# Optimization experiments

Measured on AMD Instinct MI355X. Metric: run time of the kernel, lower is better.

## Reference

```python
import jax, jax.numpy as jnp
import numpy as np

T, HID, H, KV, D = 2048, 2048, 16, 8, 128
EPS = 1e-6
THETA = 10000.0


def setup_inputs() -> dict:
    key = jax.random.key(0)
    ks = jax.random.split(key, 6)
    positions = jnp.arange(T, dtype=jnp.int64 if jax.config.jax_enable_x64 else jnp.int32)
    hidden_states = jax.random.normal(ks[0], (T, HID), dtype=jnp.float32)
    scale = 0.02
    Wq = jax.random.normal(ks[1], (HID, H * 2 * D), dtype=jnp.float32) * scale
    Wk = jax.random.normal(ks[2], (HID, KV * D), dtype=jnp.float32) * scale
    Wv = jax.random.normal(ks[3], (HID, KV * D), dtype=jnp.float32) * scale
    Wo = jax.random.normal(ks[4], (H * D, HID), dtype=jnp.float32) * scale
    q_norm_w = jnp.zeros((D,), dtype=jnp.float32)  # torch init: zeros, applied as (1+w)
    k_norm_w = jnp.zeros((D,), dtype=jnp.float32)
    return {"positions": positions, "hidden_states": hidden_states, "Wq": Wq,
            "Wk": Wk, "Wv": Wv, "Wo": Wo, "q_norm_w": q_norm_w, "k_norm_w": k_norm_w}


def _rms_norm(x, w):
    # fp32 RMSNorm with (1 + weight) scaling, per last dim
    xf = x.astype(jnp.float32)
    inv = jax.lax.rsqrt(jnp.mean(xf * xf, axis=-1, keepdims=True) + EPS)
    return (xf * inv * (1.0 + w.astype(jnp.float32))).astype(x.dtype)


def _rope(x, positions):
    # neox-style rotary over full head_dim; x: (T, heads, D)
    half = D // 2
    inv_freq = 1.0 / (THETA ** (jnp.arange(0, half, dtype=jnp.float32) / half))
    freqs = positions.astype(jnp.float32)[:, None] * inv_freq  # (T, half)
    cos = jnp.cos(freqs)[:, None, :]  # (T,1,half)
    sin = jnp.sin(freqs)[:, None, :]
    x1, x2 = x[..., :half], x[..., half:]
    return jnp.concatenate([x1 * cos - x2 * sin, x2 * cos + x1 * sin], axis=-1)


def reference(positions, hidden_states, Wq, Wk, Wv, Wo, q_norm_w, k_norm_w):
    scaling = D ** -0.5
    qg = (hidden_states @ Wq).reshape(T, H, 2 * D)
    q, gate = qg[..., :D], qg[..., D:]              # (T,H,D) each
    k = (hidden_states @ Wk).reshape(T, KV, D)
    v = (hidden_states @ Wv).reshape(T, KV, D)
    q = _rms_norm(q, q_norm_w)
    k = _rms_norm(k, k_norm_w)
    q = _rope(q, positions)
    k = _rope(k, positions)
    # GQA: repeat kv heads
    rep = H // KV
    k = jnp.repeat(k, rep, axis=1)                   # (T,H,D)
    v = jnp.repeat(v, rep, axis=1)
    scores = jnp.einsum('thd,shd->hts', q, k) * scaling  # (H,T,T)
    causal = positions[:, None] >= positions[None, :]     # (T,T)
    scores = jnp.where(causal[None], scores, jnp.finfo(scores.dtype).min)
    probs = jax.nn.softmax(scores, axis=-1)
    o = jnp.einsum('hts,shd->thd', probs, v).reshape(T, H * D)
    o = o * jax.nn.sigmoid(gate.reshape(T, H * D))
    return o @ Wo
```

## Files before the change

kernel.cpp:

```cpp
#include <hip/hip_runtime.h>
#include <stdint.h>
#include <math.h>

#define T_SEQ 2048
#define HID   2048
#define NH    16
#define NKV   8
#define DH    128

typedef __bf16 bf16x8 __attribute__((ext_vector_type(8)));
typedef float  f32x4  __attribute__((ext_vector_type(4)));

__device__ __forceinline__ ushort f2bf(float f) {
  uint32_t u = __float_as_uint(f);
  u += 0x7FFF + ((u >> 16) & 1);
  return (ushort)(u >> 16);
}
__device__ __forceinline__ ushort f2bf_rz(float f) {
  return (ushort)(__float_as_uint(f) >> 16);
}
__device__ __forceinline__ float bf2f(ushort u) {
  return __uint_as_float(((uint32_t)u) << 16);
}
__device__ __forceinline__ void gld16(const void* g, void* l) {
  __builtin_amdgcn_global_load_lds(
      (const __attribute__((address_space(1))) uint32_t*)g,
      (__attribute__((address_space(3))) uint32_t*)l, 16, 0, 0);
}

__global__ __launch_bounds__(256) void prep_kernel(
    const float* __restrict__ hs, const float* __restrict__ Wq,
    const float* __restrict__ Wk, const float* __restrict__ Wv,
    const float* __restrict__ Wo, ushort* __restrict__ hs16,
    ushort* __restrict__ Wqt, ushort* __restrict__ Wkt,
    ushort* __restrict__ Wvt, ushort* __restrict__ Wot) {
  int bid = blockIdx.x;
  if (bid < 4096) {
    int i = (bid * 256 + threadIdx.x) * 4;
    float4 v = *(const float4*)(hs + i);
    ushort4 o = {f2bf(v.x), f2bf(v.y), f2bf(v.z), f2bf(v.w)};
    *(ushort4*)(hs16 + i) = o;
    return;
  }
  bid -= 4096;
  const float* src; ushort* dst; int N, bi, bj;
  if (bid < 2048)      { src = Wq; dst = Wqt; N = 4096; bj = bid & 63; bi = bid >> 6; }
  else if (bid < 2560) { bid -= 2048; src = Wk; dst = Wkt; N = 1024; bj = bid & 15; bi = bid >> 4; }
  else if (bid < 3072) { bid -= 2560; src = Wv; dst = Wvt; N = 1024; bj = bid & 15; bi = bid >> 4; }
  else                 { bid -= 3072; src = Wo; dst = Wot; N = 2048; bj = bid & 31; bi = bid >> 5; }
  __shared__ float tile[64][65];
  const int r = threadIdx.x >> 2, cg = (threadIdx.x & 3) * 16;
  const float* sp = src + (size_t)(bi * 64 + r) * N + bj * 64 + cg;
#pragma unroll
  for (int p = 0; p < 4; ++p) {
    float4 v = *(const float4*)(sp + p * 4);
    tile[r][cg + p * 4 + 0] = v.x; tile[r][cg + p * 4 + 1] = v.y;
    tile[r][cg + p * 4 + 2] = v.z; tile[r][cg + p * 4 + 3] = v.w;
  }
  __syncthreads();
  ushort* dp = dst + (size_t)(bj * 64 + r) * HID + bi * 64 + cg;
#pragma unroll
  for (int p = 0; p < 2; ++p) {
    union { uint4 v; ushort u[8]; } o;
#pragma unroll
    for (int j = 0; j < 8; ++j) o.u[j] = f2bf(tile[cg + p * 8 + j][r]);
    *(uint4*)(dp + p * 8) = o.v;
  }
}

template <int MI>
__device__ __forceinline__ void gemm_loop(
    const ushort* __restrict__ A, const ushort* __restrict__ Bt,
    int K, int m0, int n0, ushort* As, ushort* Bs, f32x4 (*acc)[4]) {
  const int tid = threadIdx.x, lane = tid & 63, w = tid >> 6;
  const int quad = lane >> 4, l15 = lane & 15;
  const int wm = (w >> 1) * (MI * 16), wn = (w & 1) * 64;
  const int srow = tid >> 2, sch = tid & 3;
  for (int k0 = 0; k0 < K; k0 += 32) {
    __syncthreads();
#pragma unroll
    for (int p = 0; p < MI / 2; ++p) {
      int row = p * 64 + srow;
      int gch = sch ^ ((row >> 1) & 3);
      gld16(A + (size_t)(m0 + row) * K + k0 + gch * 8,
            As + (p * 256 + w * 64) * 8);
    }
#pragma unroll
    for (int p = 0; p < 2; ++p) {
      int row = p * 64 + srow;
      int gch = sch ^ ((row >> 1) & 3);
      gld16(Bt + (size_t)(n0 + row) * K + k0 + gch * 8,
            Bs + (p * 256 + w * 64) * 8);
    }
    __syncthreads();
    bf16x8 af[MI], bfr[4];
#pragma unroll
    for (int mi = 0; mi < MI; ++mi) {
      int row = wm + mi * 16 + l15;
      int pch = quad ^ ((row >> 1) & 3);
      af[mi] = *(const bf16x8*)(As + row * 32 + pch * 8);
    }
#pragma unroll
    for (int ni = 0; ni < 4; ++ni) {
      int row = wn + ni * 16 + l15;
      int pch = quad ^ ((row >> 1) & 3);
      bfr[ni] = *(const bf16x8*)(Bs + row * 32 + pch * 8);
    }
#pragma unroll
    for (int mi = 0; mi < MI; ++mi)
#pragma unroll
      for (int ni = 0; ni < 4; ++ni)
        acc[mi][ni] = __builtin_amdgcn_mfma_f32_16x16x32_bf16(
            af[mi], bfr[ni], acc[mi][ni], 0, 0, 0);
  }
}

__device__ __forceinline__ void bf16_store(f32x4 (*acc)[4],
                                           ushort* __restrict__ Cb, int Ncols,
                                           int m0, int n0) {
  const int lane = threadIdx.x & 63, w = threadIdx.x >> 6;
  const int quad = lane >> 4, l15 = lane & 15;
  const int wm = (w >> 1) * 64, wn = (w & 1) * 64;
#pragma unroll
  for (int mi = 0; mi < 4; ++mi)
#pragma unroll
    for (int ni = 0; ni < 4; ++ni)
#pragma unroll
      for (int r = 0; r < 4; ++r) {
        int row = m0 + wm + mi * 16 + quad * 4 + r;
        int col = n0 + wn + ni * 16 + l15;
        Cb[(size_t)row * Ncols + col] = f2bf(acc[mi][ni][r]);
      }
}

struct SmemQKV {
  union {
    struct { ushort As[128 * 32]; ushort Bs[128 * 32]; } g;
    struct { ushort qn[128][132]; float rss[128][2]; } n;
  };
};

__device__ __forceinline__ void norm_rope_store(
    f32x4 (*acc)[4], ushort* __restrict__ dst, int nheads, int m0, int head,
    const int* __restrict__ positions, const float* __restrict__ wgt,
    SmemQKV* sm) {
  const int tid = threadIdx.x, lane = tid & 63, w = tid >> 6;
  const int quad = lane >> 4, l15 = lane & 15;
  const int wm = (w >> 1) * 64, wn = (w & 1) * 64;
  __syncthreads();
#pragma unroll
  for (int mi = 0; mi < 4; ++mi)
#pragma unroll
    for (int r = 0; r < 4; ++r) {
      const int row = wm + mi * 16 + quad * 4 + r;
      float ss = 0.f;
#pragma unroll
      for (int ni = 0; ni < 4; ++ni) {
        float v = acc[mi][ni][r];
        ss += v * v;
        sm->n.qn[row][wn + ni * 16 + l15] = f2bf(v);
      }
      ss += __shfl_xor(ss, 8, 64);
      ss += __shfl_xor(ss, 4, 64);
      ss += __shfl_xor(ss, 2, 64);
      ss += __shfl_xor(ss, 1, 64);
      if (l15 == 0) sm->n.rss[row][w & 1] = ss;
    }
  __syncthreads();
  const int row = tid >> 1, d0 = (tid & 1) * 32;
  const int t = m0 + row;
  const float rstd =
      rsqrtf((sm->n.rss[row][0] + sm->n.rss[row][1]) * (1.f / 128.f) + 1e-6f);
  const float pos = (float)positions[t];
  ushort o1[32], o2[32];
#pragma unroll
  for (int j = 0; j < 32; ++j) {
    const int d = d0 + j;
    float x1 = bf2f(sm->n.qn[row][d]) * rstd * (1.f + wgt[d]);
    float x2 = bf2f(sm->n.qn[row][d + 64]) * rstd * (1.f + wgt[d + 64]);
    float rev = pos * exp2f((float)d * -0.20762050593045233f) *
                0.15915494309189535f;
    float fr = rev - floorf(rev);
    float s = __builtin_amdgcn_sinf(fr);
    float c = __builtin_amdgcn_cosf(fr);
    o1[j] = f2bf(x1 * c - x2 * s);
    o2[j] = f2bf(x2 * c + x1 * s);
  }
  ushort* op = dst + ((size_t)t * nheads + head) * DH;
#pragma unroll
  for (int p = 0; p < 4; ++p)
    *(uint4*)(op + d0 + p * 8) = *(const uint4*)(o1 + p * 8);
#pragma unroll
  for (int p = 0; p < 4; ++p)
    *(uint4*)(op + 64 + d0 + p * 8) = *(const uint4*)(o2 + p * 8);
}

__global__ __launch_bounds__(256) void gemm_qkv(
    const ushort* __restrict__ hs16, const ushort* __restrict__ Wqt,
    const ushort* __restrict__ Wkt, const ushort* __restrict__ Wvt,
    const int* __restrict__ positions, const float* __restrict__ qnw,
    const float* __restrict__ knw, ushort* __restrict__ q16,
    ushort* __restrict__ gate16, ushort* __restrict__ k16,
    ushort* __restrict__ v16t) {
  __shared__ alignas(16) SmemQKV sm;
  f32x4 acc[4][4];
#pragma unroll
  for (int i = 0; i < 4; ++i)
#pragma unroll
    for (int j = 0; j < 4; ++j) acc[i][j] = (f32x4){0.f, 0.f, 0.f, 0.f};
  const int b = blockIdx.x;
  if (b < 512) {
    int mt = b >> 5, nt = b & 31, m0 = mt * 128;
    gemm_loop<4>(hs16, Wqt, HID, m0, nt * 128, sm.g.As, sm.g.Bs, acc);
    if ((nt & 1) == 0)
      norm_rope_store(acc, q16, NH, m0, nt >> 1, positions, qnw, &sm);
    else
      bf16_store(acc, gate16, NH * DH, m0, (nt >> 1) * 128);
  } else if (b < 640) {
    int f = b - 512, m0 = (f >> 3) * 128, n0 = (f & 7) * 128;
    gemm_loop<4>(hs16, Wkt, HID, m0, n0, sm.g.As, sm.g.Bs, acc);
    norm_rope_store(acc, k16, NKV, m0, n0 >> 7, positions, knw, &sm);
  } else {
    int f = b - 640, m0 = (f >> 4) * 128, n0 = (f & 15) * 128;
    gemm_loop<4>(Wvt, hs16, HID, m0, n0, sm.g.As, sm.g.Bs, acc);
    bf16_store(acc, v16t, T_SEQ, m0, n0);
  }
}

__global__ __launch_bounds__(256) void gemm_out(
    const ushort* __restrict__ ob16, const ushort* __restrict__ Wot,
    float* __restrict__ out) {
  __shared__ ushort As[64 * 32];
  __shared__ ushort Bs[128 * 32];
  f32x4 acc[2][4];
#pragma unroll
  for (int i = 0; i < 2; ++i)
#pragma unroll
    for (int j = 0; j < 4; ++j) acc[i][j] = (f32x4){0.f, 0.f, 0.f, 0.f};
  const int b = blockIdx.x;
  const int m0 = (b >> 4) * 64, n0 = (b & 15) * 128;
  gemm_loop<2>(ob16, Wot, HID, m0, n0, As, Bs, acc);
  const int lane = threadIdx.x & 63, w = threadIdx.x >> 6;
  const int quad = lane >> 4, l15 = lane & 15;
  const int wm = (w >> 1) * 32, wn = (w & 1) * 64;
#pragma unroll
  for (int mi = 0; mi < 2; ++mi)
#pragma unroll
    for (int ni = 0; ni < 4; ++ni)
#pragma unroll
      for (int r = 0; r < 4; ++r) {
        int row = m0 + wm + mi * 16 + quad * 4 + r;
        int col = n0 + wn + ni * 16 + l15;
        out[(size_t)row * HID + col] = acc[mi][ni][r];
      }
}

__global__ __launch_bounds__(256) void attn_mfma(
    const ushort* __restrict__ q16, const ushort* __restrict__ k16,
    const ushort* __restrict__ v16t, const float* __restrict__ qnw,
    const float* __restrict__ knw, ushort* __restrict__ Op0,
    ushort* __restrict__ Op1, ushort* __restrict__ Op2,
    float* __restrict__ lpart) {
  const int pb = blockIdx.x, h = blockIdx.y, s = blockIdx.z, kvh = h >> 1;
  const int tid = threadIdx.x, lane = tid & 63, w = tid >> 6;
  const int quad = lane >> 4, l15 = lane & 15;

  __shared__ ushort Ks[64 * 128];
  __shared__ ushort Vs[144 * 64];
  __shared__ ushort Ps[4][16][72];

  for (int i = tid; i < 16 * 64; i += 256) {
    int row = 128 + (i >> 6), col = i & 63;
    Vs[row * 64 + col] = (row == 128) ? (ushort)0x3F80 : (ushort)0;
  }

  __shared__ float s8[8];
  __shared__ float bshare;
  {
    float mq = 0.f, mk = 0.f;
    if (tid < 128) { mq = fabsf(1.f + qnw[tid]); mk = fabsf(1.f + knw[tid]); }
#pragma unroll
    for (int off = 32; off >= 1; off >>= 1) {
      mq = fmaxf(mq, __shfl_xor(mq, off, 64));
      mk = fmaxf(mk, __shfl_xor(mk, off, 64));
    }
    if (lane == 0) { s8[w * 2] = mq; s8[w * 2 + 1] = mk; }
    __syncthreads();
    if (tid == 0) {
      float MQ = fmaxf(s8[0], s8[2]), MK = fmaxf(s8[1], s8[3]);
      bshare = 16.3217f * MQ * MK * 1.02f + 0.1f;
    }
    __syncthreads();
  }
  const float B = bshare;
  const float CSC = 0.08838834764831845f * 1.44269504088896f;

#pragma unroll 1
  for (int sel = 0; sel < 2; ++sel) {
    const int qt = sel ? (31 - pb) : pb;
    const int q0 = qt * 64;
    const int ntl = (qt >= s) ? ((qt - s) / 3 + 1) : 0;

    bf16x8 qf[4];
    const ushort* qbase = q16 + ((size_t)(q0 + w * 16 + l15) * NH + h) * DH;
#pragma unroll
    for (int ks = 0; ks < 4; ++ks)
      qf[ks] = *(const bf16x8*)(qbase + ks * 32 + quad * 8);

    f32x4 oacc[9];
#pragma unroll
    for (int i = 0; i < 9; ++i) oacc[i] = (f32x4){0.f, 0.f, 0.f, 0.f};

#pragma unroll 1
    for (int it = 0; it < ntl; ++it) {
      const int kt = s + 3 * it;
      const int kt0 = kt * 64;
      __syncthreads();
#pragma unroll
      for (int p = 0; p < 4; ++p) {
        int row = p * 16 + (tid >> 4), ch = tid & 15;
        int gch = ch ^ (row & 15);
        gld16(k16 + ((size_t)(kt0 + row) * NKV + kvh) * DH + gch * 8,
              Ks + (p * 256 + w * 64) * 8);
      }
#pragma unroll
      for (int p = 0; p < 4; ++p) {
        int row = p * 32 + (tid >> 3), ch = tid & 7;
        int gch = ch ^ (row & 7);
        gld16(v16t + (size_t)(kvh * DH + row) * T_SEQ + kt0 + gch * 8,
              Vs + (p * 256 + w * 64) * 8);
      }
      __syncthreads();

      f32x4 sacc[4];
#pragma unroll
      for (int ni = 0; ni < 4; ++ni) sacc[ni] = (f32x4){0.f, 0.f, 0.f, 0.f};
#pragma unroll
      for (int ks = 0; ks < 4; ++ks)
#pragma unroll
        for (int ni = 0; ni < 4; ++ni) {
          int row = ni * 16 + l15;
          int pch = (ks * 4 + quad) ^ (row & 15);
          bf16x8 kf = *(const bf16x8*)(Ks + row * 128 + pch * 8);
          sacc[ni] = __builtin_amdgcn_mfma_f32_16x16x32_bf16(
              qf[ks], kf, sacc[ni], 0, 0, 0);
        }

      const bool diag = (kt == qt);
#pragma unroll
      for (int ni = 0; ni < 4; ++ni) {
        int key = kt0 + ni * 16 + l15;
#pragma unroll
        for (int r = 0; r < 4; ++r) {
          float arg = fmaf(sacc[ni][r], CSC, -B);
          float pv;
          if (diag) {
            int q = q0 + w * 16 + quad * 4 + r;
            pv = (key <= q) ? exp2f(arg) : 0.f;
          } else {
            pv = exp2f(arg);
          }
          Ps[w][quad * 4 + r][ni * 16 + l15] = f2bf_rz(pv);
        }
      }

#pragma unroll
      for (int ks2 = 0; ks2 < 2; ++ks2) {
        bf16x8 pf = *(const bf16x8*)(&Ps[w][l15][ks2 * 32 + quad * 8]);
#pragma unroll
        for (int ni = 0; ni < 9; ++ni) {
          int row = ni * 16 + l15;
          int pch = (ks2 * 4 + quad) ^ (row & 7);
          bf16x8 vf = *(const bf16x8*)(Vs + row * 64 + pch * 8);
          oacc[ni] = __builtin_amdgcn_mfma_f32_16x16x32_bf16(
              pf, vf, oacc[ni], 0, 0, 0);
        }
      }
    }

    ushort* Op = (s == 0) ? Op0 : (s == 1) ? Op1 : Op2;
#pragma unroll
    for (int ni = 0; ni < 8; ++ni) {
      int d = ni * 16 + l15;
#pragma unroll
      for (int r = 0; r < 4; ++r) {
        int q = q0 + w * 16 + quad * 4 + r;
        Op[((size_t)h * T_SEQ + q) * DH + d] = f2bf(oacc[ni][r]);
      }
    }
    if (l15 == 0) {
#pragma unroll
      for (int r = 0; r < 4; ++r) {
        int q = q0 + w * 16 + quad * 4 + r;
        lpart[(size_t)s * (NH * T_SEQ) + h * T_SEQ + q] = oacc[8][r];
      }
    }
  }
}

__global__ __launch_bounds__(256) void combine_kernel(
    const ushort* __restrict__ Op0, const ushort* __restrict__ Op1,
    const ushort* __restrict__ Op2, const float* __restrict__ lpart,
    const ushort* __restrict__ gate16, ushort* __restrict__ ob16) {
  const int t = blockIdx.x, tid = threadIdx.x;
  const int h = tid >> 4, d0 = (tid & 15) * 8;
  const int NT = NH * T_SEQ;
  const float l = lpart[h * T_SEQ + t] + lpart[NT + h * T_SEQ + t] +
                  lpart[2 * NT + h * T_SEQ + t];
  const float inv = 1.0f / l;
  const size_t po = ((size_t)h * T_SEQ + t) * DH + d0;
  ushort4 a0 = *(const ushort4*)(Op0 + po);
  ushort4 a1 = *(const ushort4*)(Op0 + po + 4);
  ushort4 b0 = *(const ushort4*)(Op1 + po);
  ushort4 b1 = *(const ushort4*)(Op1 + po + 4);
  ushort4 c0 = *(const ushort4*)(Op2 + po);
  ushort4 c1 = *(const ushort4*)(Op2 + po + 4);
  const ushort* gp = gate16 + (size_t)t * (NH * DH) + h * DH + d0;
  ushort4 g0 = *(const ushort4*)(gp);
  ushort4 g1 = *(const ushort4*)(gp + 4);
  float oa[8] = {bf2f(a0.x), bf2f(a0.y), bf2f(a0.z), bf2f(a0.w),
                 bf2f(a1.x), bf2f(a1.y), bf2f(a1.z), bf2f(a1.w)};
  float ob[8] = {bf2f(b0.x), bf2f(b0.y), bf2f(b0.z), bf2f(b0.w),
                 bf2f(b1.x), bf2f(b1.y), bf2f(b1.z), bf2f(b1.w)};
  float oc[8] = {bf2f(c0.x), bf2f(c0.y), bf2f(c0.z), bf2f(c0.w),
                 bf2f(c1.x), bf2f(c1.y), bf2f(c1.z), bf2f(c1.w)};
  float gg[8] = {bf2f(g0.x), bf2f(g0.y), bf2f(g0.z), bf2f(g0.w),
                 bf2f(g1.x), bf2f(g1.y), bf2f(g1.z), bf2f(g1.w)};
  ushort r[8];
#pragma unroll
  for (int i = 0; i < 8; ++i) {
    float o = (oa[i] + ob[i] + oc[i]) * inv;
    o = o / (1.0f + exp2f(-gg[i] * 1.44269504088896f));
    r[i] = f2bf(o);
  }
  ushort* op = ob16 + (size_t)t * (NH * DH) + h * DH + d0;
  *(ushort4*)(op)     = (ushort4){r[0], r[1], r[2], r[3]};
  *(ushort4*)(op + 4) = (ushort4){r[4], r[5], r[6], r[7]};
}

extern "C" void kernel_launch(void* const* d_in, const int* in_sizes, int n_in,
                              void* d_out, int out_size, void* d_ws, size_t ws_size,
                              hipStream_t stream) {
  const int*   positions = (const int*)d_in[0];
  const float* hs  = (const float*)d_in[1];
  const float* Wq  = (const float*)d_in[2];
  const float* Wk  = (const float*)d_in[3];
  const float* Wv  = (const float*)d_in[4];
  const float* Wo  = (const float*)d_in[5];
  const float* qnw = (const float*)d_in[6];
  const float* knw = (const float*)d_in[7];
  float* out = (float*)d_out;

  const size_t MB = 1 << 20;
  uint8_t* ws = (uint8_t*)d_ws;
  ushort* hs16  = (ushort*)(ws + 0);
  ushort* Op0   = (ushort*)(ws + 0);
  ushort* Wqt   = (ushort*)(ws + 8 * MB);
  ushort* Op1   = (ushort*)(ws + 8 * MB);
  ushort* Op2   = (ushort*)(ws + 16 * MB);
  ushort* Wkt   = (ushort*)(ws + 24 * MB);
  ushort* ob16  = (ushort*)(ws + 24 * MB);
  ushort* Wvt   = (ushort*)(ws + 28 * MB);
  ushort* v16t  = (ushort*)(ws + 32 * MB);
  ushort* k16   = (ushort*)(ws + 36 * MB);
  ushort* q16   = (ushort*)(ws + 40 * MB);
  ushort* gate16= (ushort*)(ws + 48 * MB);
  ushort* Wot   = (ushort*)(ws + 56 * MB);
  float*  lpart = (float*)d_out;

  prep_kernel<<<8192, 256, 0, stream>>>(hs, Wq, Wk, Wv, Wo,
                                        hs16, Wqt, Wkt, Wvt, Wot);
  gemm_qkv<<<768, 256, 0, stream>>>(hs16, Wqt, Wkt, Wvt, positions, qnw, knw,
                                    q16, gate16, k16, v16t);
  attn_mfma<<<dim3(16, NH, 3), 256, 0, stream>>>(q16, k16, v16t, qnw, knw,
                                                 Op0, Op1, Op2, lpart);
  combine_kernel<<<T_SEQ, 256, 0, stream>>>(Op0, Op1, Op2, lpart, gate16, ob16);
  gemm_out<<<512, 256, 0, stream>>>(ob16, Wot, out);
}
```

Measured before the change: 291.4 us.

## Fuse RMSNorm+RoPE in registers via 4x1 warp tiling; widen out-GEMM K tile

The Q/K projection GEMM now uses a 4x1 warp layout, so each wave holds whole 128-wide head rows. RMSNorm and RoPE can then run directly in registers with 16-lane shuffles, with no shared-memory staging and no extra block barriers. The output GEMM gets its own inline loop with a 64-wide K tile and XOR swizzle, halving the barrier count per K. Costs: each wave reloads the full B tile per k-step (less reuse), stores become scattered 2-byte writes instead of 16-byte vector writes, and shared memory for gemm_out grows.

```diff
diff --git a/kernel.cpp b/kernel.cpp
--- a/kernel.cpp
+++ b/kernel.cpp
@@ -133,66 +133,111 @@
       }
 }
 
-struct SmemQKV {
-  union {
-    struct { ushort As[128 * 32]; ushort Bs[128 * 32]; } g;
-    struct { ushort qn[128][132]; float rss[128][2]; } n;
-  };
-};
-
-__device__ __forceinline__ void norm_rope_store(
-    f32x4 (*acc)[4], ushort* __restrict__ dst, int nheads, int m0, int head,
-    const int* __restrict__ positions, const float* __restrict__ wgt,
-    SmemQKV* sm) {
+__device__ __forceinline__ void gemm_loop41(
+    const ushort* __restrict__ A, const ushort* __restrict__ Bt,
+    int K, int m0, int n0, ushort* As, ushort* Bs, f32x4 (*acc)[8]) {
   const int tid = threadIdx.x, lane = tid & 63, w = tid >> 6;
   const int quad = lane >> 4, l15 = lane & 15;
-  const int wm = (w >> 1) * 64, wn = (w & 1) * 64;
-  __syncthreads();
-#pragma unroll
-  for (int mi = 0; mi < 4; ++mi)
+  const int srow = tid >> 2, sch = tid & 3;
+  for (int k0 = 0; k0 < K; k0 += 32) {
+    __syncthreads();
+#pragma unroll
+    for (int p = 0; p < 2; ++p) {
+      int row = p * 64 + srow;
+      int gch = sch ^ ((row >> 1) & 3);
+      gld16(A + (size_t)(m0 + row) * K + k0 + gch * 8,
+            As + (p * 256 + w * 64) * 8);
+    }
+#pragma unroll
+    for (int p = 0; p < 2; ++p) {
+      int row = p * 64 + srow;
+      int gch = sch ^ ((row >> 1) & 3);
+      gld16(Bt + (size_t)(n0 + row) * K + k0 + gch * 8,
+            Bs + (p * 256 + w * 64) * 8);
+    }
+    __syncthreads();
+    bf16x8 af[2];
+#pragma unroll
+    for (int mi = 0; mi < 2; ++mi) {
+      int row = w * 32 + mi * 16 + l15;
+      int pch = quad ^ ((row >> 1) & 3);
+      af[mi] = *(const bf16x8*)(As + row * 32 + pch * 8);
+    }
+#pragma unroll
+    for (int ni = 0; ni < 8; ++ni) {
+      int row = ni * 16 + l15;
+      int pch = quad ^ ((row >> 1) & 3);
+      bf16x8 bfr = *(const bf16x8*)(Bs + row * 32 + pch * 8);
+      acc[0][ni] = __builtin_amdgcn_mfma_f32_16x16x32_bf16(
+          af[0], bfr, acc[0][ni], 0, 0, 0);
+      acc[1][ni] = __builtin_amdgcn_mfma_f32_16x16x32_bf16(
+          af[1], bfr, acc[1][ni], 0, 0, 0);
+    }
+  }
+}
+
+__device__ __forceinline__ void store41_plain(f32x4 (*acc)[8],
+                                              ushort* __restrict__ Cb,
+                                              int Ncols, int m0, int n0) {
+  const int lane = threadIdx.x & 63, w = threadIdx.x >> 6;
+  const int quad = lane >> 4, l15 = lane & 15;
+#pragma unroll
+  for (int mi = 0; mi < 2; ++mi)
+#pragma unroll
+    for (int ni = 0; ni < 8; ++ni)
+#pragma unroll
+      for (int r = 0; r < 4; ++r) {
+        int row = m0 + w * 32 + mi * 16 + quad * 4 + r;
+        int col = n0 + ni * 16 + l15;
+        Cb[(size_t)row * Ncols + col] = f2bf(acc[mi][ni][r]);
+      }
+}
+
+__device__ __forceinline__ void store41_normrope(
+    f32x4 (*acc)[8], ushort* __restrict__ dst, int ncols, int m0, int colbase,
+    const int* __restrict__ positions, const float* __restrict__ wgt) {
+  const int lane = threadIdx.x & 63, w = threadIdx.x >> 6;
+  const int quad = lane >> 4, l15 = lane & 15;
+  float wv[8], invc[4];
+#pragma unroll
+  for (int ni = 0; ni < 8; ++ni) wv[ni] = 1.f + wgt[ni * 16 + l15];
+#pragma unroll
+  for (int ni = 0; ni < 4; ++ni)
+    invc[ni] = exp2f((float)(ni * 16 + l15) * -0.20762050593045233f) *
+               0.15915494309189535f;
+#pragma unroll
+  for (int mi = 0; mi < 2; ++mi)
 #pragma unroll
     for (int r = 0; r < 4; ++r) {
-      const int row = wm + mi * 16 + quad * 4 + r;
+      const int row = m0 + w * 32 + mi * 16 + quad * 4 + r;
       float ss = 0.f;
 #pragma unroll
-      for (int ni = 0; ni < 4; ++ni) {
+      for (int ni = 0; ni < 8; ++ni) {
         float v = acc[mi][ni][r];
         ss += v * v;
-        sm->n.qn[row][wn + ni * 16 + l15] = f2bf(v);
-      }
-      ss += __shfl_xor(ss, 8, 64);
-      ss += __shfl_xor(ss, 4, 64);
-      ss += __shfl_xor(ss, 2, 64);
-      ss += __shfl_xor(ss, 1, 64);
-      if (l15 == 0) sm->n.rss[row][w & 1] = ss;
-    }
-  __syncthreads();
-  const int row = tid >> 1, d0 = (tid & 1) * 32;
-  const int t = m0 + row;
-  const float rstd =
-      rsqrtf((sm->n.rss[row][0] + sm->n.rss[row][1]) * (1.f / 128.f) + 1e-6f);
-  const float pos = (float)positions[t];
-  ushort o1[32], o2[32];
-#pragma unroll
-  for (int j = 0; j < 32; ++j) {
-    const int d = d0 + j;
-    float x1 = bf2f(sm->n.qn[row][d]) * rstd * (1.f + wgt[d]);
-    float x2 = bf2f(sm->n.qn[row][d + 64]) * rstd * (1.f + wgt[d + 64]);
-    float rev = pos * exp2f((float)d * -0.20762050593045233f) *
-                0.15915494309189535f;
-    float fr = rev - floorf(rev);
-    float s = __builtin_amdgcn_sinf(fr);
-    float c = __builtin_amdgcn_cosf(fr);
-    o1[j] = f2bf(x1 * c - x2 * s);
-    o2[j] = f2bf(x2 * c + x1 * s);
-  }
-  ushort* op = dst + ((size_t)t * nheads + head) * DH;
-#pragma unroll
-  for (int p = 0; p < 4; ++p)
-    *(uint4*)(op + d0 + p * 8) = *(const uint4*)(o1 + p * 8);
-#pragma unroll
-  for (int p = 0; p < 4; ++p)
-    *(uint4*)(op + 64 + d0 + p * 8) = *(const uint4*)(o2 + p * 8);
+      }
+      ss += __shfl_xor(ss, 1, 16);
+      ss += __shfl_xor(ss, 2, 16);
+      ss += __shfl_xor(ss, 4, 16);
+      ss += __shfl_xor(ss, 8, 16);
+      const float rstd = rsqrtf(ss * (1.f / 128.f) + 1e-6f);
+      const float pos = (float)positions[row];
+      ushort o[8];
+#pragma unroll
+      for (int ni = 0; ni < 4; ++ni) {
+        float x1 = acc[mi][ni][r] * rstd * wv[ni];
+        float x2 = acc[mi][ni + 4][r] * rstd * wv[ni + 4];
+        float rev = pos * invc[ni];
+        float fr = rev - floorf(rev);
+        float s = __builtin_amdgcn_sinf(fr);
+        float c = __builtin_amdgcn_cosf(fr);
+        o[ni]     = f2bf(x1 * c - x2 * s);
+        o[ni + 4] = f2bf(x2 * c + x1 * s);
+      }
+      ushort* op = dst + (size_t)row * ncols + colbase;
+#pragma unroll
+      for (int ni = 0; ni < 8; ++ni) op[ni * 16 + l15] = o[ni];
+    }
 }
 
 __global__ __launch_bounds__(256) void gemm_qkv(
@@ -202,27 +247,36 @@
     const float* __restrict__ knw, ushort* __restrict__ q16,
     ushort* __restrict__ gate16, ushort* __restrict__ k16,
     ushort* __restrict__ v16t) {
-  __shared__ alignas(16) SmemQKV sm;
-  f32x4 acc[4][4];
-#pragma unroll
-  for (int i = 0; i < 4; ++i)
-#pragma unroll
-    for (int j = 0; j < 4; ++j) acc[i][j] = (f32x4){0.f, 0.f, 0.f, 0.f};
+  __shared__ ushort As[128 * 32];
+  __shared__ ushort Bs[128 * 32];
   const int b = blockIdx.x;
-  if (b < 512) {
-    int mt = b >> 5, nt = b & 31, m0 = mt * 128;
-    gemm_loop<4>(hs16, Wqt, HID, m0, nt * 128, sm.g.As, sm.g.Bs, acc);
-    if ((nt & 1) == 0)
-      norm_rope_store(acc, q16, NH, m0, nt >> 1, positions, qnw, &sm);
-    else
-      bf16_store(acc, gate16, NH * DH, m0, (nt >> 1) * 128);
-  } else if (b < 640) {
-    int f = b - 512, m0 = (f >> 3) * 128, n0 = (f & 7) * 128;
-    gemm_loop<4>(hs16, Wkt, HID, m0, n0, sm.g.As, sm.g.Bs, acc);
-    norm_rope_store(acc, k16, NKV, m0, n0 >> 7, positions, knw, &sm);
+  if (b < 640) {
+    f32x4 acc[2][8];
+#pragma unroll
+    for (int i = 0; i < 2; ++i)
+#pragma unroll
+      for (int j = 0; j < 8; ++j) acc[i][j] = (f32x4){0.f, 0.f, 0.f, 0.f};
+    if (b < 512) {
+      int mt = b >> 5, nt = b & 31, m0 = mt * 128;
+      gemm_loop41(hs16, Wqt, HID, m0, nt * 128, As, Bs, acc);
+      if ((nt & 1) == 0)
+        store41_normrope(acc, q16, NH * DH, m0, (nt >> 1) * 128, positions,
+                         qnw);
+      else
+        store41_plain(acc, gate16, NH * DH, m0, (nt >> 1) * 128);
+    } else {
+      int f = b - 512, m0 = (f >> 3) * 128, n0 = (f & 7) * 128;
+      gemm_loop41(hs16, Wkt, HID, m0, n0, As, Bs, acc);
+      store41_normrope(acc, k16, 1024, m0, n0, positions, knw);
+    }
   } else {
+    f32x4 acc[4][4];
+#pragma unroll
+    for (int i = 0; i < 4; ++i)
+#pragma unroll
+      for (int j = 0; j < 4; ++j) acc[i][j] = (f32x4){0.f, 0.f, 0.f, 0.f};
     int f = b - 640, m0 = (f >> 4) * 128, n0 = (f & 15) * 128;
-    gemm_loop<4>(Wvt, hs16, HID, m0, n0, sm.g.As, sm.g.Bs, acc);
+    gemm_loop<4>(Wvt, hs16, HID, m0, n0, As, Bs, acc);
     bf16_store(acc, v16t, T_SEQ, m0, n0);
   }
 }
@@ -230,8 +284,8 @@
 __global__ __launch_bounds__(256) void gemm_out(
     const ushort* __restrict__ ob16, const ushort* __restrict__ Wot,
     float* __restrict__ out) {
-  __shared__ ushort As[64 * 32];
-  __shared__ ushort Bs[128 * 32];
+  __shared__ ushort As[64 * 64];
+  __shared__ ushort Bs[128 * 64];
   f32x4 acc[2][4];
 #pragma unroll
   for (int i = 0; i < 2; ++i)
@@ -239,10 +293,50 @@
     for (int j = 0; j < 4; ++j) acc[i][j] = (f32x4){0.f, 0.f, 0.f, 0.f};
   const int b = blockIdx.x;
   const int m0 = (b >> 4) * 64, n0 = (b & 15) * 128;
-  gemm_loop<2>(ob16, Wot, HID, m0, n0, As, Bs, acc);
-  const int lane = threadIdx.x & 63, w = threadIdx.x >> 6;
+  const int tid = threadIdx.x, lane = tid & 63, w = tid >> 6;
   const int quad = lane >> 4, l15 = lane & 15;
   const int wm = (w >> 1) * 32, wn = (w & 1) * 64;
+  const int srow = tid >> 3, sch = tid & 7;
+  for (int k0 = 0; k0 < HID; k0 += 64) {
+    __syncthreads();
+#pragma unroll
+    for (int p = 0; p < 2; ++p) {
+      int row = p * 32 + srow;
+      int gch = sch ^ (row & 7);
+      gld16(ob16 + (size_t)(m0 + row) * HID + k0 + gch * 8,
+            As + (p * 256 + w * 64) * 8);
+    }
+#pragma unroll
+    for (int p = 0; p < 4; ++p) {
+      int row = p * 32 + srow;
+      int gch = sch ^ (row & 7);
+      gld16(Wot + (size_t)(n0 + row) * HID + k0 + gch * 8,
+            Bs + (p * 256 + w * 64) * 8);
+    }
+    __syncthreads();
+#pragma unroll
+    for (int ks = 0; ks < 2; ++ks) {
+      bf16x8 af[2], bfr[4];
+#pragma unroll
+      for (int mi = 0; mi < 2; ++mi) {
+        int row = wm + mi * 16 + l15;
+        int pch = (ks * 4 + quad) ^ (row & 7);
+        af[mi] = *(const bf16x8*)(As + row * 64 + pch * 8);
+      }
+#pragma unroll
+      for (int ni = 0; ni < 4; ++ni) {
+        int row = wn + ni * 16 + l15;
+        int pch = (ks * 4 + quad) ^ (row & 7);
+        bfr[ni] = *(const bf16x8*)(Bs + row * 64 + pch * 8);
+      }
+#pragma unroll
+      for (int mi = 0; mi < 2; ++mi)
+#pragma unroll
+        for (int ni = 0; ni < 4; ++ni)
+          acc[mi][ni] = __builtin_amdgcn_mfma_f32_16x16x32_bf16(
+              af[mi], bfr[ni], acc[mi][ni], 0, 0, 0);
+    }
+  }
 #pragma unroll
   for (int mi = 0; mi < 2; ++mi)
 #pragma unroll
```

Result: faster. 285.1 us (-2.1%).
